# Optimization experiments

Hardware: AMD Instinct MI355X
Metric: run time of the kernel (lower is better)

## Reference

```python
import jax, jax.numpy as jnp
import numpy as np

N, E, B = 16000, 256000, 32
IN, HID, H1, OUT, H2 = 768, 256, 4, 128, 2
LN_EPS = 1e-5


def _gat_layer(x, src, dst, W, a_src, a_dst, b, heads, out, n, concat):
    # x: (n, in), W: (heads*out, in), a_src/a_dst: (heads, out), b: (heads*out,) or (out,)
    h = (x @ W.T).reshape(n, heads, out)                      # (n, H, out)
    alpha_s = (h * a_src).sum(-1)                             # (n, H)
    alpha_d = (h * a_dst).sum(-1)                             # (n, H)
    e = jax.nn.leaky_relu(alpha_s[src] + alpha_d[dst], 0.2)   # (E', H)
    # segment softmax over incoming edges of each dst node
    m = jax.ops.segment_max(e, dst, num_segments=n)           # (n, H)
    ex = jnp.exp(e - m[dst])
    den = jax.ops.segment_sum(ex, dst, num_segments=n)
    alpha = ex / (den[dst] + 1e-16)                           # (E', H)
    msg = h[src] * alpha[..., None]                           # (E', H, out)
    agg = jax.ops.segment_sum(msg, dst, num_segments=n)       # (n, H, out)
    o = agg.reshape(n, heads * out) if concat else agg.mean(axis=1)
    return o + b


def setup_inputs() -> dict:
    key = jax.random.key(0)
    ks = jax.random.split(key, 16)
    x = jax.random.normal(ks[0], (N, IN), dtype=jnp.float32)
    edge_index = jax.random.randint(ks[1], (2, E), 0, N, dtype=jnp.int32)
    batch = jnp.sort(jax.random.randint(ks[2], (N,), 0, B, dtype=jnp.int32))
    s = 0.05
    return {
        "x": x, "edge_index": edge_index, "batch": batch,
        "W1": jax.random.normal(ks[3], (H1 * HID, IN), jnp.float32) * s,
        "a1_src": jax.random.normal(ks[4], (H1, HID), jnp.float32) * s,
        "a1_dst": jax.random.normal(ks[5], (H1, HID), jnp.float32) * s,
        "b1": jnp.zeros((H1 * HID,), jnp.float32),
        "W2": jax.random.normal(ks[6], (H2 * OUT, H1 * HID), jnp.float32) * s,
        "a2_src": jax.random.normal(ks[7], (H2, OUT), jnp.float32) * s,
        "a2_dst": jax.random.normal(ks[8], (H2, OUT), jnp.float32) * s,
        "b2": jnp.zeros((OUT,), jnp.float32),
        "proj_W": jax.random.normal(ks[9], (768, OUT), jnp.float32) * s,
        "proj_b": jnp.zeros((768,), jnp.float32),
        "ln_g": jnp.ones((768,), jnp.float32),
        "ln_b": jnp.zeros((768,), jnp.float32),
    }


def reference(x, edge_index, batch, W1, a1_src, a1_dst, b1,
              W2, a2_src, a2_dst, b2, proj_W, proj_b, ln_g, ln_b):
    # add self-loops (PyG GATConv default add_self_loops=True)
    loop = jnp.arange(N, dtype=edge_index.dtype)
    src = jnp.concatenate([edge_index[0], loop])
    dst = jnp.concatenate([edge_index[1], loop])

    h1 = jax.nn.elu(_gat_layer(x, src, dst, W1, a1_src, a1_dst, b1, H1, HID, N, True))
    # dropout = 0 (eval mode)
    h2 = jax.nn.elu(_gat_layer(h1, src, dst, W2, a2_src, a2_dst, b2, H2, OUT, N, False))

    # global mean pool per graph
    sums = jax.ops.segment_sum(h2, batch, num_segments=B)            # (B, OUT)
    cnt = jax.ops.segment_sum(jnp.ones((N,), h2.dtype), batch, num_segments=B)
    pooled = sums / jnp.maximum(cnt, 1.0)[:, None]

    z = pooled @ proj_W.T + proj_b                                   # (B, 768)
    mu = z.mean(-1, keepdims=True)
    var = ((z - mu) ** 2).mean(-1, keepdims=True)
    graph_embed = (z - mu) / jnp.sqrt(var + LN_EPS) * ln_g + ln_b
    return graph_embed, h2
```

## Files before the change

kernel.cpp:

```cpp
#include <hip/hip_runtime.h>
#include <cstddef>

#define NN   16000
#define NE   256000
#define EP   (NE + NN)
#define BG   32
#define IN_F 768
#define HID  256
#define H1C  4
#define F1   (H1C * HID)
#define OUTF 128
#define H2C  2
#define F2   (H2C * OUTF)

typedef __bf16 bf16x8 __attribute__((ext_vector_type(8)));
typedef float  f32x4  __attribute__((ext_vector_type(4)));
typedef float  f32x2  __attribute__((ext_vector_type(2)));
typedef unsigned short us8 __attribute__((ext_vector_type(8)));
typedef unsigned short us4 __attribute__((ext_vector_type(4)));

static __device__ __forceinline__ float lrelu02(float x) { return x > 0.f ? x : 0.2f * x; }
static __device__ __forceinline__ float eluf(float x)    { return x > 0.f ? x : expm1f(x); }
static __device__ __forceinline__ unsigned short rne_bf16(float f) {
    unsigned u = __float_as_uint(f);
    return (unsigned short)((u + 0x7fffu + ((u >> 16) & 1u)) >> 16);
}
static __device__ __forceinline__ f32x2 cvt2(unsigned int u) {
    f32x2 r;
    r.x = __uint_as_float(u << 16);
    r.y = __uint_as_float(u & 0xffff0000u);
    return r;
}

#define GLDS16(gp, lp) __builtin_amdgcn_global_load_lds(                         \
    (const __attribute__((address_space(1))) void*)(gp),                          \
    (__attribute__((address_space(3))) void*)(lp), 16, 0, 0)

#define NB_X  ((NN * IN_F) / 1024)
#define NB_W1 ((F1 * IN_F) / 1024)
#define NB_W2 ((F2 * F1) / 1024)
#define NB_H  ((EP + 255) / 256)
#define NB_PREP (NB_X + NB_W1 + NB_W2 + NB_H)

static __device__ __forceinline__ void f2b_body(const float* __restrict__ in,
                                                unsigned short* __restrict__ out,
                                                int blk, int t) {
    int i = (blk * 256 + t) * 4;
    float4 v = *(const float4*)&in[i];
    ushort4 o;
    o.x = rne_bf16(v.x); o.y = rne_bf16(v.y); o.z = rne_bf16(v.z); o.w = rne_bf16(v.w);
    *(ushort4*)&out[i] = o;
}

__global__ __launch_bounds__(256) void k_prep(const float* __restrict__ x,
                                              const float* __restrict__ W1,
                                              const float* __restrict__ W2,
                                              unsigned short* __restrict__ xb,
                                              unsigned short* __restrict__ W1b,
                                              unsigned short* __restrict__ W2b,
                                              const int* __restrict__ ei,
                                              int* __restrict__ deg) {
    int b = blockIdx.x, t = threadIdx.x;
    if (b < NB_X) { f2b_body(x, xb, b, t); return; }
    b -= NB_X;
    if (b < NB_W1) { f2b_body(W1, W1b, b, t); return; }
    b -= NB_W1;
    if (b < NB_W2) { f2b_body(W2, W2b, b, t); return; }
    b -= NB_W2;
    int e = b * 256 + t;
    if (e >= EP) return;
    int d = (e < NE) ? ei[NE + e] : (e - NE);
    atomicAdd(&deg[d], 1);
}

__global__ __launch_bounds__(1024) void k_scan(const int* __restrict__ deg,
                                               int* __restrict__ off, int* __restrict__ cursor) {
    __shared__ int sums[1024];
    int t = threadIdx.x;
    const int CH = 16;
    int base = t * CH;
    int s = 0;
    for (int i = 0; i < CH; ++i) { int idx = base + i; if (idx < NN) s += deg[idx]; }
    sums[t] = s;
    __syncthreads();
    for (int ofs = 1; ofs < 1024; ofs <<= 1) {
        int v = 0;
        if (t >= ofs) v = sums[t - ofs];
        __syncthreads();
        sums[t] += v;
        __syncthreads();
    }
    int run = sums[t] - s;
    for (int i = 0; i < CH; ++i) {
        int idx = base + i;
        if (idx < NN) { off[idx] = run; cursor[idx] = run; run += deg[idx]; }
    }
    if (t == 1023) off[NN] = run;
}

template <int KITER, int HSHIFT, int HCNT>
static __device__ __forceinline__ void gemm_body(const unsigned short* __restrict__ A,
                                                 const unsigned short* __restrict__ B,
                                                 unsigned short* __restrict__ C,
                                                 const float* __restrict__ a_s,
                                                 const float* __restrict__ a_d,
                                                 float* __restrict__ as_o,
                                                 float* __restrict__ ad_o,
                                                 int N, int K, int bx, int by,
                                                 unsigned short* As, unsigned short* Bs,
                                                 int t) {
    const int w = t >> 6, lane = t & 63;
    const int m0 = by * 128, n0 = bx * 128;
    const int wm = (w >> 1) * 64, wn = (w & 1) * 64;

    const unsigned short* ga0 = A + (size_t)(m0 + (t >> 2)) * K + (t & 3) * 8;
    const unsigned short* ga1 = ga0 + (size_t)64 * K;
    const unsigned short* gb0 = B + (size_t)(n0 + (t >> 2)) * K + (t & 3) * 8;
    const unsigned short* gb1 = gb0 + (size_t)64 * K;
    unsigned short* lA0 = &As[(w * 64) * 8];
    unsigned short* lA1 = &As[(w * 64 + 256) * 8];
    unsigned short* lB0 = &Bs[(w * 64) * 8];
    unsigned short* lB1 = &Bs[(w * 64 + 256) * 8];

    f32x4 acc[4][4] = {};

    const bf16x8* pa = (const bf16x8*)As + (wm + (lane & 15)) * 4 + (lane >> 4);
    const bf16x8* pb = (const bf16x8*)Bs + (wn + (lane & 15)) * 4 + (lane >> 4);

    for (int it = 0; it < KITER; ++it) {
        GLDS16(ga0, lA0); GLDS16(ga1, lA1);
        GLDS16(gb0, lB0); GLDS16(gb1, lB1);
        ga0 += 32; ga1 += 32; gb0 += 32; gb1 += 32;
        __syncthreads();
        bf16x8 a0 = pa[0], a1 = pa[64], a2 = pa[128], a3 = pa[192];
        bf16x8 b0 = pb[0], b1 = pb[64], b2 = pb[128], b3 = pb[192];
        acc[0][0] = __builtin_amdgcn_mfma_f32_16x16x32_bf16(a0, b0, acc[0][0], 0, 0, 0);
        acc[0][1] = __builtin_amdgcn_mfma_f32_16x16x32_bf16(a0, b1, acc[0][1], 0, 0, 0);
        acc[0][2] = __builtin_amdgcn_mfma_f32_16x16x32_bf16(a0, b2, acc[0][2], 0, 0, 0);
        acc[0][3] = __builtin_amdgcn_mfma_f32_16x16x32_bf16(a0, b3, acc[0][3], 0, 0, 0);
        acc[1][0] = __builtin_amdgcn_mfma_f32_16x16x32_bf16(a1, b0, acc[1][0], 0, 0, 0);
        acc[1][1] = __builtin_amdgcn_mfma_f32_16x16x32_bf16(a1, b1, acc[1][1], 0, 0, 0);
        acc[1][2] = __builtin_amdgcn_mfma_f32_16x16x32_bf16(a1, b2, acc[1][2], 0, 0, 0);
        acc[1][3] = __builtin_amdgcn_mfma_f32_16x16x32_bf16(a1, b3, acc[1][3], 0, 0, 0);
        acc[2][0] = __builtin_amdgcn_mfma_f32_16x16x32_bf16(a2, b0, acc[2][0], 0, 0, 0);
        acc[2][1] = __builtin_amdgcn_mfma_f32_16x16x32_bf16(a2, b1, acc[2][1], 0, 0, 0);
        acc[2][2] = __builtin_amdgcn_mfma_f32_16x16x32_bf16(a2, b2, acc[2][2], 0, 0, 0);
        acc[2][3] = __builtin_amdgcn_mfma_f32_16x16x32_bf16(a2, b3, acc[2][3], 0, 0, 0);
        acc[3][0] = __builtin_amdgcn_mfma_f32_16x16x32_bf16(a3, b0, acc[3][0], 0, 0, 0);
        acc[3][1] = __builtin_amdgcn_mfma_f32_16x16x32_bf16(a3, b1, acc[3][1], 0, 0, 0);
        acc[3][2] = __builtin_amdgcn_mfma_f32_16x16x32_bf16(a3, b2, acc[3][2], 0, 0, 0);
        acc[3][3] = __builtin_amdgcn_mfma_f32_16x16x32_bf16(a3, b3, acc[3][3], 0, 0, 0);
        __syncthreads();
    }
    const int ccol = n0 + wn + (lane & 15);
    const int crow = m0 + wm + (lane >> 4) * 4;
#pragma unroll
    for (int mi = 0; mi < 4; ++mi)
#pragma unroll
        for (int i = 0; i < 4; ++i) {
            unsigned short* cp = C + (size_t)(crow + mi * 16 + i) * N + ccol;
            cp[0]  = rne_bf16(acc[mi][0][i]);
            cp[16] = rne_bf16(acc[mi][1][i]);
            cp[32] = rne_bf16(acc[mi][2][i]);
            cp[48] = rne_bf16(acc[mi][3][i]);
        }
    const int hh = n0 >> HSHIFT;
    float asv[4], adv[4];
#pragma unroll
    for (int bi = 0; bi < 4; ++bi) {
        asv[bi] = a_s[ccol + bi * 16];
        adv[bi] = a_d[ccol + bi * 16];
    }
#pragma unroll
    for (int mi = 0; mi < 4; ++mi)
#pragma unroll
        for (int i = 0; i < 4; ++i) {
            float vs = acc[mi][0][i] * asv[0] + acc[mi][1][i] * asv[1]
                     + acc[mi][2][i] * asv[2] + acc[mi][3][i] * asv[3];
            float vd = acc[mi][0][i] * adv[0] + acc[mi][1][i] * adv[1]
                     + acc[mi][2][i] * adv[2] + acc[mi][3][i] * adv[3];
#pragma unroll
            for (int m = 1; m <= 8; m <<= 1) {
                vs += __shfl_xor(vs, m);
                vd += __shfl_xor(vd, m);
            }
            if ((lane & 15) == 0) {
                int r = crow + mi * 16 + i;
                atomicAdd(&as_o[r * HCNT + hh], vs);
                atomicAdd(&ad_o[r * HCNT + hh], vd);
            }
        }
}

#define G1_BLKS 1024
__global__ __launch_bounds__(256) void k_gemm1(const unsigned short* __restrict__ A,
                                               const unsigned short* __restrict__ B,
                                               unsigned short* __restrict__ C,
                                               const float* __restrict__ a_s,
                                               const float* __restrict__ a_d,
                                               float* __restrict__ as_o,
                                               float* __restrict__ ad_o,
                                               const int* __restrict__ ei,
                                               int* __restrict__ cursor,
                                               int* __restrict__ csr_src,
                                               int* __restrict__ csr_dst) {
    __shared__ __align__(16) unsigned short As[4096];
    __shared__ __align__(16) unsigned short Bs[4096];
    int blk = blockIdx.x, t = threadIdx.x;
    if (blk < G1_BLKS) {
        int by = (blk & 7) + 8 * (blk >> 6);
        int bx = (blk >> 3) & 7;
        if (by < 125)
            gemm_body<24, 8, 4>(A, B, C, a_s, a_d, as_o, ad_o, F1, IN_F, bx, by, As, Bs, t);
        return;
    }
    int e = (blk - G1_BLKS) * 256 + t;
    if (e >= EP) return;
    int s, d;
    if (e < NE) { s = ei[e]; d = ei[NE + e]; } else { s = d = e - NE; }
    int pos = atomicAdd(&cursor[d], 1);
    csr_src[pos] = s;
    csr_dst[pos] = d;
}

__global__ __launch_bounds__(256) void k_gemm2(const unsigned short* __restrict__ A,
                                               const unsigned short* __restrict__ B,
                                               unsigned short* __restrict__ C,
                                               const float* __restrict__ a_s,
                                               const float* __restrict__ a_d,
                                               float* __restrict__ as_o,
                                               float* __restrict__ ad_o) {
    __shared__ __align__(16) unsigned short As[4096];
    __shared__ __align__(16) unsigned short Bs[4096];
    int blk = blockIdx.x, t = threadIdx.x;
    int by = (blk & 7) + 8 * (blk >> 4);
    int bx = (blk >> 3) & 1;
    if (by < 125)
        gemm_body<32, 7, 2>(A, B, C, a_s, a_d, as_o, ad_o, F2, F1, bx, by, As, Bs, t);
}

__global__ __launch_bounds__(256) void k_el1(const int* __restrict__ csr_src,
                                             const int* __restrict__ csr_dst,
                                             const float* __restrict__ as1,
                                             const float* __restrict__ ad1,
                                             unsigned short* __restrict__ el16) {
    int j = blockIdx.x * 256 + threadIdx.x;
    if (j >= EP) return;
    int s = csr_src[j], d = csr_dst[j];
    float4 av = *(const float4*)&as1[s * H1C];
    float4 dv = *(const float4*)&ad1[d * H1C];
    us4 o;
    o[0] = rne_bf16(expf(lrelu02(av.x + dv.x)));
    o[1] = rne_bf16(expf(lrelu02(av.y + dv.y)));
    o[2] = rne_bf16(expf(lrelu02(av.z + dv.z)));
    o[3] = rne_bf16(expf(lrelu02(av.w + dv.w)));
    *(us4*)&el16[(size_t)j * 4] = o;
}

__global__ __launch_bounds__(256) void k_el2(const int* __restrict__ csr_src,
                                             const int* __restrict__ csr_dst,
                                             const float* __restrict__ as2,
                                             const float* __restrict__ ad2,
                                             float* __restrict__ el) {
    int j = blockIdx.x * 256 + threadIdx.x;
    if (j >= EP) return;
    int s = csr_src[j], d = csr_dst[j];
    float2 av = *(const float2*)&as2[s * 2];
    float2 dv = *(const float2*)&ad2[d * 2];
    float2 o;
    o.x = expf(lrelu02(av.x + dv.x));
    o.y = expf(lrelu02(av.y + dv.y));
    *(float2*)&el[(size_t)j * 2] = o;
}

#define ISSUE1(CH, BUF, DV, EV)                                                   \
    {   int slot_ = beg + (CH) * 32 + lA;                                         \
        int sc_ = slot_ < end ? slot_ : end - 1;                                  \
        DV = (slot_ < end) ? csrd[sc_] : -1;                                      \
        EV = (int)el16[(size_t)sc_ * 4 + h];                                      \
        _Pragma("unroll")                                                         \
        for (int cc = 0; cc < 8; ++cc) {                                          \
            int slot2_ = beg + (CH) * 32 + cc * 4 + slot_in;                      \
            int sc3_ = slot2_ < end ? slot2_ : end - 1;                           \
            GLDS16(hb + (size_t)csr[sc3_] * F1 + gfeat,                           \
                   (BUF) + cc * 1024 + (cc >> 1) * 64);                           \
        } }

#define STEP1(CH, BUF, DV, EV)                                                    \
    {   if ((CH) + 1 < nch) asm volatile("s_waitcnt vmcnt(16)" ::: "memory");     \
        else                asm volatile("s_waitcnt vmcnt(0)" ::: "memory");      \
        us8 au;                                                                   \
        _Pragma("unroll")                                                         \
        for (int j = 0; j < 8; ++j) {                                             \
            int dvj = __shfl(DV, g * 8 + j);                                      \
            int evj = __shfl(EV, g * 8 + j);                                      \
            au[j] = (dvj == d0 + c) ? (unsigned short)evj : (unsigned short)0;    \
        }                                                                         \
        bf16x8 af = *(bf16x8*)&au;                                                \
        const char* rbc_ = (BUF) + g * 2112 + u * 4 + (odd ? 0 : 32);             \
        uint4 qq[8];                                                              \
        _Pragma("unroll")                                                         \
        for (int fb = 0; fb < 8; ++fb) {                                          \
            const unsigned* p = (const unsigned*)(rbc_ + fb * 128);               \
            unsigned W0 = p[0], W1 = p[16], W2 = p[256], W3 = p[272];             \
            unsigned X0 = (unsigned)__builtin_amdgcn_mov_dpp((int)W0, 0xB1, 0xF, 0xF, true); \
            unsigned X1 = (unsigned)__builtin_amdgcn_mov_dpp((int)W1, 0xB1, 0xF, 0xF, true); \
            unsigned X2 = (unsigned)__builtin_amdgcn_mov_dpp((int)W2, 0xB1, 0xF, 0xF, true); \
            unsigned X3 = (unsigned)__builtin_amdgcn_mov_dpp((int)W3, 0xB1, 0xF, 0xF, true); \
            qq[fb].x = __builtin_amdgcn_perm(W0, X0, sel);                        \
            qq[fb].y = __builtin_amdgcn_perm(W1, X1, sel);                        \
            qq[fb].z = __builtin_amdgcn_perm(W2, X2, sel);                        \
            qq[fb].w = __builtin_amdgcn_perm(W3, X3, sel);                        \
        }                                                                         \
        asm volatile("s_waitcnt lgkmcnt(0)" ::: "memory");                        \
        __builtin_amdgcn_sched_barrier(0);                                       \
        if ((CH) + 2 < nch) ISSUE1((CH) + 2, BUF, DV, EV);                        \
        dacc = __builtin_amdgcn_mfma_f32_16x16x32_bf16(af, ones, dacc, 0, 0, 0);  \
        _Pragma("unroll")                                                         \
        for (int fb = 0; fb < 8; ++fb) {                                          \
            bf16x8 bfv = *(bf16x8*)&qq[fb];                                       \
            acc[fb] = __builtin_amdgcn_mfma_f32_16x16x32_bf16(af, bfv, acc[fb], 0, 0, 0); \
        } }

__global__ __launch_bounds__(128) void k_gat1(const unsigned short* __restrict__ hb,
                                              const unsigned short* __restrict__ el16,
                                              const int* __restrict__ off,
                                              const int* __restrict__ csr,
                                              const int* __restrict__ csrd,
                                              const float* __restrict__ b1,
                                              unsigned short* __restrict__ h1b) {
    __shared__ __align__(16) char sbuf[2][2][8384];
    const int t = threadIdx.x, l = t & 63, w = t >> 6;
    const int s = blockIdx.x & 7;
    const int db = (blockIdx.x >> 3) * 2 + w;
    const int d0 = db * 16;
    const int h = s >> 1;
    const int g = l >> 4, c = l & 15;
    const int u = c >> 1, odd = c & 1;
    const int beg = off[d0], end = off[d0 + 16];
    char* buf0 = sbuf[w][0];
    char* buf1 = sbuf[w][1];
    const unsigned sel = odd ? 0x03020706u : 0x05040100u;
    const int gfeat = s * 128 + (l >> 3) * 16 + (l & 1) * 8;
    const int slot_in = (l >> 1) & 3;
    const int lA = l & 31;

    f32x4 acc[8] = {};
    f32x4 dacc = {};
    us8 onesu = {0x3F80, 0x3F80, 0x3F80, 0x3F80, 0x3F80, 0x3F80, 0x3F80, 0x3F80};
    bf16x8 ones = *(bf16x8*)&onesu;

    const int nch = (end - beg + 31) >> 5;
    int dv0, ev0, dv1 = -1, ev1 = 0;
    ISSUE1(0, buf0, dv0, ev0);
    asm volatile("" ::: "memory");
    if (nch > 1) ISSUE1(1, buf1, dv1, ev1);
    for (int ch = 0; ch < nch; ch += 2) {
        STEP1(ch, buf0, dv0, ev0);
        if (ch + 1 < nch) STEP1(ch + 1, buf1, dv1, ev1);
    }
    float rdh[4];
#pragma unroll
    for (int i = 0; i < 4; ++i) rdh[i] = 1.f / (dacc[i] + 1e-16f);
#pragma unroll
    for (int fb = 0; fb < 8; ++fb) {
        int f = s * 128 + fb * 16 + c;
        float bias = b1[f];
#pragma unroll
        for (int i = 0; i < 4; ++i) {
            int r = d0 + g * 4 + i;
            float v = eluf(acc[fb][i] * rdh[i] + bias);
            h1b[(size_t)r * F1 + f] = rne_bf16(v);
        }
    }
}

__global__ __launch_bounds__(256) void k_gat2(const unsigned short* __restrict__ h2b,
                                              const float* __restrict__ el,
                                              const int* __restrict__ off,
                                              const int* __restrict__ csr,
                                              const float* __restrict__ b2,
                                              float* __restrict__ out_h2) {
    const int l = threadIdx.x & 63;
    const int d = blockIdx.x * 4 + (threadIdx.x >> 6);
    const int beg = off[d], end = off[d + 1];
    const int c = l & 31, p = l >> 5;
    const int myhead = c >> 4;
    const int hw = p;

    float s0 = 0.f, s1 = 0.f;
    for (int j = beg + l; j < end; j += 64) {
        float2 e = *(const float2*)&el[(size_t)j * 2];
        s0 += e.x; s1 += e.y;
    }
    for (int o = 32; o > 0; o >>= 1) {
        s0 += __shfl_down(s0, o);
        s1 += __shfl_down(s1, o);
    }
    s0 = __shfl(s0, 0); s1 = __shfl(s1, 0);
    float rdhw = 1.f / ((hw ? s1 : s0) + 1e-16f);

    f32x2 acc[4] = {};
    const unsigned int* base = (const unsigned int*)h2b + c * 4;
    for (int cbeg = beg; cbeg < end; cbeg += 32) {
        int cnt = end - cbeg; if (cnt > 32) cnt = 32;
        int idx = cbeg + c;
        int idxc = idx < end ? idx : end - 1;
        int s_sel = csr[idxc];
        float ev = el[(size_t)idxc * 2 + hw];
        float myw = (idx < end) ? ev * rdhw : 0.f;
        for (int jj = 0; jj < cnt; jj += 8) {
            int e0 = jj + p * 4;
            int sa = __shfl(s_sel, e0 + 0);
            int sb = __shfl(s_sel, e0 + 1);
            int sc = __shfl(s_sel, e0 + 2);
            int sd = __shfl(s_sel, e0 + 3);
            float wa = __shfl(myw, (myhead << 5) | (e0 + 0));
            float wb = __shfl(myw, (myhead << 5) | (e0 + 1));
            float wc = __shfl(myw, (myhead << 5) | (e0 + 2));
            float wd = __shfl(myw, (myhead << 5) | (e0 + 3));
            uint4 va = *(const uint4*)(base + (unsigned)sa * (F2 / 2));
            uint4 vb = *(const uint4*)(base + (unsigned)sb * (F2 / 2));
            uint4 vc = *(const uint4*)(base + (unsigned)sc * (F2 / 2));
            uint4 vd = *(const uint4*)(base + (unsigned)sd * (F2 / 2));
            f32x2 wa2 = {wa, wa}, wb2 = {wb, wb}, wc2 = {wc, wc}, wd2 = {wd, wd};
            acc[0] += wa2 * cvt2(va.x); acc[1] += wa2 * cvt2(va.y);
            acc[2] += wa2 * cvt2(va.z); acc[3] += wa2 * cvt2(va.w);
            acc[0] += wb2 * cvt2(vb.x); acc[1] += wb2 * cvt2(vb.y);
            acc[2] += wb2 * cvt2(vb.z); acc[3] += wb2 * cvt2(vb.w);
            acc[0] += wc2 * cvt2(vc.x); acc[1] += wc2 * cvt2(vc.y);
            acc[2] += wc2 * cvt2(vc.z); acc[3] += wc2 * cvt2(vc.w);
            acc[0] += wd2 * cvt2(vd.x); acc[1] += wd2 * cvt2(vd.y);
            acc[2] += wd2 * cvt2(vd.z); acc[3] += wd2 * cvt2(vd.w);
        }
    }
    float af[8] = {acc[0].x, acc[0].y, acc[1].x, acc[1].y,
                   acc[2].x, acc[2].y, acc[3].x, acc[3].y};
#pragma unroll
    for (int i = 0; i < 8; ++i) af[i] += __shfl(af[i], l ^ 32);
    float pt[8];
#pragma unroll
    for (int i = 0; i < 8; ++i) pt[i] = __shfl(af[i], l ^ 16);
    if (l < 16) {
        int f = l * 8;
        float o[8];
#pragma unroll
        for (int i = 0; i < 8; ++i) o[i] = eluf(0.5f * (af[i] + pt[i]) + b2[f + i]);
        *(float4*)&out_h2[(size_t)d * OUTF + f]     = make_float4(o[0], o[1], o[2], o[3]);
        *(float4*)&out_h2[(size_t)d * OUTF + f + 4] = make_float4(o[4], o[5], o[6], o[7]);
    }
}

__global__ __launch_bounds__(1024) void k_proj_ln(const float* __restrict__ h2,
                                                  const int* __restrict__ batch,
                                                  const float* __restrict__ pW,
                                                  const float* __restrict__ pb,
                                                  const float* __restrict__ g,
                                                  const float* __restrict__ be,
                                                  float* __restrict__ out) {
    __shared__ float part[1024];
    __shared__ float ph[OUTF];
    __shared__ float zb[768];
    __shared__ float red[1024];
    __shared__ float s_mu, s_rstd;
    int b = blockIdx.x, t = threadIdx.x;
    int lo = 0, hi = NN;
    while (lo < hi) { int mid = (lo + hi) >> 1; if (batch[mid] < b) lo = mid + 1; else hi = mid; }
    int n0 = lo;
    lo = 0; hi = NN;
    while (lo < hi) { int mid = (lo + hi) >> 1; if (batch[mid] < b + 1) lo = mid + 1; else hi = mid; }
    int n1 = lo;
    {
        int f = t & 127, slot = t >> 7;
        float a = 0.f;
        for (int n = n0 + slot; n < n1; n += 8) a += h2[(size_t)n * OUTF + f];
        part[t] = a;
    }
    __syncthreads();
    if (t < OUTF) {
        float s = 0.f;
#pragma unroll
        for (int k = 0; k < 8; ++k) s += part[k * 128 + t];
        float c = (float)(n1 - n0);
        c = c < 1.f ? 1.f : c;
        ph[t] = s / c;
    }
    __syncthreads();
    if (t < 768) {
        float acc = pb[t];
        for (int k = 0; k < OUTF; k += 4) {
            float4 w = *(const float4*)&pW[(size_t)t * OUTF + k];
            acc += w.x * ph[k] + w.y * ph[k + 1] + w.z * ph[k + 2] + w.w * ph[k + 3];
        }
        zb[t] = acc;
    }
    __syncthreads();
    red[t] = (t < 768) ? zb[t] : 0.f;
    __syncthreads();
    for (int ofs = 512; ofs > 0; ofs >>= 1) {
        if (t < ofs) red[t] += red[t + ofs];
        __syncthreads();
    }
    if (t == 0) s_mu = red[0] / 768.f;
    __syncthreads();
    float mu = s_mu;
    float dv = (t < 768) ? (zb[t] - mu) : 0.f;
    red[t] = dv * dv;
    __syncthreads();
    for (int ofs = 512; ofs > 0; ofs >>= 1) {
        if (t < ofs) red[t] += red[t + ofs];
        __syncthreads();
    }
    if (t == 0) s_rstd = rsqrtf(red[0] / 768.f + 1e-5f);
    __syncthreads();
    float rstd = s_rstd;
    if (t < 768)
        out[(size_t)b * 768 + t] = (zb[t] - mu) * rstd * g[t] + be[t];
}

extern "C" void kernel_launch(void* const* d_in, const int* in_sizes, int n_in,
                              void* d_out, int out_size, void* d_ws, size_t ws_size,
                              hipStream_t stream) {
    const float* x    = (const float*)d_in[0];
    const int*   ei   = (const int*)d_in[1];
    const int*   batch= (const int*)d_in[2];
    const float* W1   = (const float*)d_in[3];
    const float* a1s  = (const float*)d_in[4];
    const float* a1d  = (const float*)d_in[5];
    const float* b1   = (const float*)d_in[6];
    const float* W2   = (const float*)d_in[7];
    const float* a2s  = (const float*)d_in[8];
    const float* a2d  = (const float*)d_in[9];
    const float* b2   = (const float*)d_in[10];
    const float* pW   = (const float*)d_in[11];
    const float* pb   = (const float*)d_in[12];
    const float* lng  = (const float*)d_in[13];
    const float* lnb  = (const float*)d_in[14];

    float* out_ge = (float*)d_out;
    float* out_h2 = (float*)d_out + BG * 768;

    char* w = (char*)d_ws;
    unsigned short* xb   = (unsigned short*)w;  w += (size_t)NN * IN_F * 2;
    unsigned short* W1b  = (unsigned short*)w;  w += (size_t)F1 * IN_F * 2;
    unsigned short* W2b  = (unsigned short*)w;  w += (size_t)F2 * F1 * 2;
    unsigned short* hbufb= (unsigned short*)w;  w += (size_t)NN * F1 * 2;
    unsigned short* h1b  = (unsigned short*)w;  w += (size_t)NN * F1 * 2;
    unsigned short* h2b  = (unsigned short*)w;  w += (size_t)NN * F2 * 2;
    float* as1  = (float*)w;  w += (size_t)NN * H1C * 4;
    float* ad1  = (float*)w;  w += (size_t)NN * H1C * 4;
    float* as2  = (float*)w;  w += (size_t)NN * H2C * 4;
    float* ad2  = (float*)w;  w += (size_t)NN * H2C * 4;
    int* deg    = (int*)w;    w += (size_t)NN * 4;
    int* off    = (int*)w;    w += (size_t)(NN + 4) * 4;
    int* cursor = (int*)w;    w += (size_t)NN * 4;
    int* csr    = (int*)w;    w += (size_t)EP * 4;
    int* csrd   = (int*)w;    w += (size_t)EP * 4;
    unsigned short* el16 = (unsigned short*)w;  w += (size_t)EP * H1C * 2;
    float* el2  = (float*)w;  w += (size_t)EP * H2C * 4;

    hipMemsetAsync(as1, 0, (size_t)NN * (H1C + H1C + H2C + H2C + 1) * 4, stream);

    k_prep<<<NB_PREP, 256, 0, stream>>>(x, W1, W2, xb, W1b, W2b, ei, deg);
    k_scan<<<1, 1024, 0, stream>>>(deg, off, cursor);

    k_gemm1<<<G1_BLKS + NB_H, 256, 0, stream>>>(xb, W1b, hbufb, a1s, a1d, as1, ad1,
                                                ei, cursor, csr, csrd);
    k_el1<<<(EP + 255) / 256, 256, 0, stream>>>(csr, csrd, as1, ad1, el16);
    k_gat1<<<4000, 128, 0, stream>>>(hbufb, el16, off, csr, csrd, b1, h1b);

    k_gemm2<<<256, 256, 0, stream>>>(h1b, W2b, h2b, a2s, a2d, as2, ad2);
    k_el2<<<(EP + 255) / 256, 256, 0, stream>>>(csr, csrd, as2, ad2, el2);
    k_gat2<<<NN / 4, 256, 0, stream>>>(h2b, el2, off, csr, b2, out_h2);

    k_proj_ln<<<BG, 1024, 0, stream>>>(out_h2, batch, pW, pb, lng, lnb, out_ge);
}
```

Before: 409.1 us.

## Double-buffer GEMM LDS tiles and swizzle LDS layout to avoid bank conflicts

The GEMM main loop now uses two LDS buffers so the global-to-LDS load of the next K-slice is issued before the MFMAs on the current slice run. This hides load latency behind compute instead of stalling on every iteration. It also XOR-swizzles the 16-byte chunk index on both the load and read side to reduce LDS bank conflicts. In exchange it doubles shared memory per block, which can lower occupancy, and it relies on KITER being even.

```diff
diff --git a/kernel.cpp b/kernel.cpp
--- a/kernel.cpp
+++ b/kernel.cpp
@@ -98,6 +98,34 @@
     if (t == 1023) off[NN] = run;
 }
 
+#define GEMM_MM16(POFS)                                                              \
+    {   bf16x8 a0 = pa[(POFS)], a1 = pa[(POFS) + 64], a2 = pa[(POFS) + 128],         \
+               a3 = pa[(POFS) + 192];                                                \
+        bf16x8 b0 = pb[(POFS)], b1 = pb[(POFS) + 64], b2 = pb[(POFS) + 128],         \
+               b3 = pb[(POFS) + 192];                                                \
+        acc[0][0] = __builtin_amdgcn_mfma_f32_16x16x32_bf16(a0, b0, acc[0][0], 0, 0, 0); \
+        acc[0][1] = __builtin_amdgcn_mfma_f32_16x16x32_bf16(a0, b1, acc[0][1], 0, 0, 0); \
+        acc[0][2] = __builtin_amdgcn_mfma_f32_16x16x32_bf16(a0, b2, acc[0][2], 0, 0, 0); \
+        acc[0][3] = __builtin_amdgcn_mfma_f32_16x16x32_bf16(a0, b3, acc[0][3], 0, 0, 0); \
+        acc[1][0] = __builtin_amdgcn_mfma_f32_16x16x32_bf16(a1, b0, acc[1][0], 0, 0, 0); \
+        acc[1][1] = __builtin_amdgcn_mfma_f32_16x16x32_bf16(a1, b1, acc[1][1], 0, 0, 0); \
+        acc[1][2] = __builtin_amdgcn_mfma_f32_16x16x32_bf16(a1, b2, acc[1][2], 0, 0, 0); \
+        acc[1][3] = __builtin_amdgcn_mfma_f32_16x16x32_bf16(a1, b3, acc[1][3], 0, 0, 0); \
+        acc[2][0] = __builtin_amdgcn_mfma_f32_16x16x32_bf16(a2, b0, acc[2][0], 0, 0, 0); \
+        acc[2][1] = __builtin_amdgcn_mfma_f32_16x16x32_bf16(a2, b1, acc[2][1], 0, 0, 0); \
+        acc[2][2] = __builtin_amdgcn_mfma_f32_16x16x32_bf16(a2, b2, acc[2][2], 0, 0, 0); \
+        acc[2][3] = __builtin_amdgcn_mfma_f32_16x16x32_bf16(a2, b3, acc[2][3], 0, 0, 0); \
+        acc[3][0] = __builtin_amdgcn_mfma_f32_16x16x32_bf16(a3, b0, acc[3][0], 0, 0, 0); \
+        acc[3][1] = __builtin_amdgcn_mfma_f32_16x16x32_bf16(a3, b1, acc[3][1], 0, 0, 0); \
+        acc[3][2] = __builtin_amdgcn_mfma_f32_16x16x32_bf16(a3, b2, acc[3][2], 0, 0, 0); \
+        acc[3][3] = __builtin_amdgcn_mfma_f32_16x16x32_bf16(a3, b3, acc[3][3], 0, 0, 0); }
+
+#define GEMM_STAGE(IT, OFS)                                                          \
+    {   const unsigned short* pA_ = ga0 + (IT) * 32;                                 \
+        const unsigned short* pB_ = gb0 + (IT) * 32;                                 \
+        GLDS16(pA_, lA0 + (OFS)); GLDS16(pA_ + K64, lA1 + (OFS));                    \
+        GLDS16(pB_, lB0 + (OFS)); GLDS16(pB_ + K64, lB1 + (OFS)); }
+
 template <int KITER, int HSHIFT, int HCNT>
 static __device__ __forceinline__ void gemm_body(const unsigned short* __restrict__ A,
                                                  const unsigned short* __restrict__ B,
@@ -113,43 +141,33 @@
     const int m0 = by * 128, n0 = bx * 128;
     const int wm = (w >> 1) * 64, wn = (w & 1) * 64;
 
-    const unsigned short* ga0 = A + (size_t)(m0 + (t >> 2)) * K + (t & 3) * 8;
-    const unsigned short* ga1 = ga0 + (size_t)64 * K;
-    const unsigned short* gb0 = B + (size_t)(n0 + (t >> 2)) * K + (t & 3) * 8;
-    const unsigned short* gb1 = gb0 + (size_t)64 * K;
-    unsigned short* lA0 = &As[(w * 64) * 8];
-    unsigned short* lA1 = &As[(w * 64 + 256) * 8];
-    unsigned short* lB0 = &Bs[(w * 64) * 8];
-    unsigned short* lB1 = &Bs[(w * 64 + 256) * 8];
+    const int qsw = (t & 3) ^ ((t >> 3) & 3);
+    const unsigned short* ga0 = A + (size_t)(m0 + (t >> 2)) * K + qsw * 8;
+    const unsigned short* gb0 = B + (size_t)(n0 + (t >> 2)) * K + qsw * 8;
+    const size_t K64 = (size_t)64 * K;
+
+    unsigned short* lA0 = &As[w * 512];
+    unsigned short* lA1 = &As[w * 512 + 2048];
+    unsigned short* lB0 = &Bs[w * 512];
+    unsigned short* lB1 = &Bs[w * 512 + 2048];
 
     f32x4 acc[4][4] = {};
 
-    const bf16x8* pa = (const bf16x8*)As + (wm + (lane & 15)) * 4 + (lane >> 4);
-    const bf16x8* pb = (const bf16x8*)Bs + (wn + (lane & 15)) * 4 + (lane >> 4);
-
-    for (int it = 0; it < KITER; ++it) {
-        GLDS16(ga0, lA0); GLDS16(ga1, lA1);
-        GLDS16(gb0, lB0); GLDS16(gb1, lB1);
-        ga0 += 32; ga1 += 32; gb0 += 32; gb1 += 32;
+    const int slot = (lane >> 4) ^ ((lane >> 1) & 3);
+    const bf16x8* pa = (const bf16x8*)As + (wm + (lane & 15)) * 4 + slot;
+    const bf16x8* pb = (const bf16x8*)Bs + (wn + (lane & 15)) * 4 + slot;
+
+    GEMM_STAGE(0, 0);
+    asm volatile("s_waitcnt vmcnt(0)" ::: "memory");
+    __syncthreads();
+    for (int it = 0; it < KITER; it += 2) {
+        GEMM_STAGE(it + 1, 4096);
+        GEMM_MM16(0);
+        asm volatile("s_waitcnt vmcnt(0)" ::: "memory");
         __syncthreads();
-        bf16x8 a0 = pa[0], a1 = pa[64], a2 = pa[128], a3 = pa[192];
-        bf16x8 b0 = pb[0], b1 = pb[64], b2 = pb[128], b3 = pb[192];
-        acc[0][0] = __builtin_amdgcn_mfma_f32_16x16x32_bf16(a0, b0, acc[0][0], 0, 0, 0);
-        acc[0][1] = __builtin_amdgcn_mfma_f32_16x16x32_bf16(a0, b1, acc[0][1], 0, 0, 0);
-        acc[0][2] = __builtin_amdgcn_mfma_f32_16x16x32_bf16(a0, b2, acc[0][2], 0, 0, 0);
-        acc[0][3] = __builtin_amdgcn_mfma_f32_16x16x32_bf16(a0, b3, acc[0][3], 0, 0, 0);
-        acc[1][0] = __builtin_amdgcn_mfma_f32_16x16x32_bf16(a1, b0, acc[1][0], 0, 0, 0);
-        acc[1][1] = __builtin_amdgcn_mfma_f32_16x16x32_bf16(a1, b1, acc[1][1], 0, 0, 0);
-        acc[1][2] = __builtin_amdgcn_mfma_f32_16x16x32_bf16(a1, b2, acc[1][2], 0, 0, 0);
-        acc[1][3] = __builtin_amdgcn_mfma_f32_16x16x32_bf16(a1, b3, acc[1][3], 0, 0, 0);
-        acc[2][0] = __builtin_amdgcn_mfma_f32_16x16x32_bf16(a2, b0, acc[2][0], 0, 0, 0);
-        acc[2][1] = __builtin_amdgcn_mfma_f32_16x16x32_bf16(a2, b1, acc[2][1], 0, 0, 0);
-        acc[2][2] = __builtin_amdgcn_mfma_f32_16x16x32_bf16(a2, b2, acc[2][2], 0, 0, 0);
-        acc[2][3] = __builtin_amdgcn_mfma_f32_16x16x32_bf16(a2, b3, acc[2][3], 0, 0, 0);
-        acc[3][0] = __builtin_amdgcn_mfma_f32_16x16x32_bf16(a3, b0, acc[3][0], 0, 0, 0);
-        acc[3][1] = __builtin_amdgcn_mfma_f32_16x16x32_bf16(a3, b1, acc[3][1], 0, 0, 0);
-        acc[3][2] = __builtin_amdgcn_mfma_f32_16x16x32_bf16(a3, b2, acc[3][2], 0, 0, 0);
-        acc[3][3] = __builtin_amdgcn_mfma_f32_16x16x32_bf16(a3, b3, acc[3][3], 0, 0, 0);
+        if (it + 2 < KITER) GEMM_STAGE(it + 2, 0);
+        GEMM_MM16(512);
+        asm volatile("s_waitcnt vmcnt(0)" ::: "memory");
         __syncthreads();
     }
     const int ccol = n0 + wn + (lane & 15);
@@ -204,8 +222,8 @@
                                                int* __restrict__ cursor,
                                                int* __restrict__ csr_src,
                                                int* __restrict__ csr_dst) {
-    __shared__ __align__(16) unsigned short As[4096];
-    __shared__ __align__(16) unsigned short Bs[4096];
+    __shared__ __align__(16) unsigned short As[8192];
+    __shared__ __align__(16) unsigned short Bs[8192];
     int blk = blockIdx.x, t = threadIdx.x;
     if (blk < G1_BLKS) {
         int by = (blk & 7) + 8 * (blk >> 6);
@@ -230,8 +248,8 @@
                                                const float* __restrict__ a_d,
                                                float* __restrict__ as_o,
                                                float* __restrict__ ad_o) {
-    __shared__ __align__(16) unsigned short As[4096];
-    __shared__ __align__(16) unsigned short Bs[4096];
+    __shared__ __align__(16) unsigned short As[8192];
+    __shared__ __align__(16) unsigned short Bs[8192];
     int blk = blockIdx.x, t = threadIdx.x;
     int by = (blk & 7) + 8 * (blk >> 4);
     int bx = (blk >> 3) & 1;
```

Result: no change. 413.1 us (+1.0%).
